# Optimization experiments

Measured on AMD Instinct MI355X. Metric: run time of the kernel, lower is better.

## Reference

```python
import jax, jax.numpy as jnp
import numpy as np

DIM = 1024
HEADS = 16
SEQ = 1024
BATCH = 4
SCALE = (DIM // HEADS) ** -0.5


def setup_inputs() -> dict:
    key = jax.random.key(0)
    ks = jax.random.split(key, 5)
    x = jax.random.normal(ks[0], (BATCH, SEQ, DIM), dtype=jnp.float32)
    # Linear weights stored [in, out]; y = x @ W + b (math-equivalent to torch Linear)
    w_qkv = jax.random.normal(ks[1], (DIM, 3 * DIM), dtype=jnp.float32) * (DIM ** -0.5)
    b_qkv = jnp.zeros((3 * DIM,), dtype=jnp.float32)
    w_proj = jax.random.normal(ks[2], (DIM, DIM), dtype=jnp.float32) * (DIM ** -0.5)
    b_proj = jnp.zeros((DIM,), dtype=jnp.float32)
    rel_table = jax.random.normal(ks[3], (2 * SEQ - 1, HEADS), dtype=jnp.float32) * 0.02
    coords = jnp.arange(SEQ)
    rel_index = (coords[:, None] - coords[None, :] + SEQ - 1).astype(jnp.int32)  # [N, N]
    return {"x": x, "w_qkv": w_qkv, "b_qkv": b_qkv, "w_proj": w_proj,
            "b_proj": b_proj, "rel_table": rel_table, "rel_index": rel_index}


def reference(x, w_qkv, b_qkv, w_proj, b_proj, rel_table, rel_index):
    B, N, C = x.shape
    H = HEADS
    hd = C // H
    qkv = (x @ w_qkv + b_qkv).reshape(B, N, 3, H, hd).transpose(2, 0, 3, 1, 4)  # [3,B,H,N,hd]
    q, k, v = qkv[0] * SCALE, qkv[1], qkv[2]
    attn = jnp.einsum('bhqe,bhke->bhqk', q, k)                 # [B,H,N,N]
    bias = rel_table[rel_index]                                 # [N,N,H] gather
    attn = attn + bias.transpose(2, 0, 1)[None]                 # add [1,H,N,N]
    attn = jax.nn.softmax(attn, axis=-1)
    # Faithful to the original einsum 'bnqk,bnqe->bnqe' (contracts k over attn only)
    out = jnp.einsum('bnqk,bnqe->bnqe', attn, v)                # [B,H,N,hd]
    out = out.transpose(0, 2, 1, 3).reshape(B, N, C)
    return out @ w_proj + b_proj
```

## Files before the change

kernel.cpp:

```cpp
#include <hip/hip_runtime.h>
#include <type_traits>


#define DIMC 1024
#define MTOT 4096

__device__ __forceinline__ unsigned short f2bf(float f) {
  unsigned u = __float_as_uint(f);
  u += 0x7FFFu + ((u >> 16) & 1u);
  return (unsigned short)(u >> 16);
}

typedef __attribute__((ext_vector_type(8))) short short8;
typedef __attribute__((ext_vector_type(4))) float floatx4;

__device__ __forceinline__ void async_copy16(const void* g, void* l) {
  __builtin_amdgcn_global_load_lds(
      (const __attribute__((address_space(1))) unsigned int*)g,
      (__attribute__((address_space(3))) unsigned int*)l,
      16, 0, 0);
}

__device__ __forceinline__ short8 cvt8(floatx4 lo, floatx4 hi) {
  unsigned r0, r1, r2, r3;
  asm("v_cvt_pk_bf16_f32 %0, %1, %2" : "=v"(r0) : "v"(lo[0]), "v"(lo[1]));
  asm("v_cvt_pk_bf16_f32 %0, %1, %2" : "=v"(r1) : "v"(lo[2]), "v"(lo[3]));
  asm("v_cvt_pk_bf16_f32 %0, %1, %2" : "=v"(r2) : "v"(hi[0]), "v"(hi[1]));
  asm("v_cvt_pk_bf16_f32 %0, %1, %2" : "=v"(r3) : "v"(hi[2]), "v"(hi[3]));
  union { unsigned u[4]; short8 s; } u;
  u.u[0] = r0; u.u[1] = r1; u.u[2] = r2; u.u[3] = r3;
  return u.s;
}

__global__ void prep_kernel(const float* __restrict__ w_proj,
                            const float* __restrict__ w_qkv,
                            const float* __restrict__ b_v,
                            unsigned short* __restrict__ WpT,
                            unsigned short* __restrict__ Wvb,
                            float* __restrict__ b_cp) {
  __shared__ float tile[32][33];
  const int t = threadIdx.x;
  const int tx = t & 31, ty = t >> 5;
  const int bx = blockIdx.x, by = blockIdx.y;
#pragma unroll
  for (int r = 0; r < 4; ++r) {
    int kl = ty + r * 8;
    tile[kl][tx] = w_proj[(size_t)(by * 32 + kl) * DIMC + bx * 32 + tx];
  }
  {
    const int r2 = t >> 3, c4 = (t & 7) * 4;
    float4 f = *(const float4*)(w_qkv + (size_t)(by * 32 + r2) * (3 * DIMC) +
                                2 * DIMC + bx * 32 + c4);
    ushort4 o;
    o.x = f2bf(f.x); o.y = f2bf(f.y); o.z = f2bf(f.z); o.w = f2bf(f.w);
    *(ushort4*)(Wvb + (size_t)(by * 32 + r2) * DIMC + bx * 32 + c4) = o;
  }
  __syncthreads();
#pragma unroll
  for (int r = 0; r < 4; ++r) {
    int nl = ty + r * 8;
    WpT[(size_t)(bx * 32 + nl) * DIMC + by * 32 + tx] = f2bf(tile[tx][nl]);
  }
  if (t < 32) {
    float s = 0.f;
#pragma unroll
    for (int kl = 0; kl < 32; ++kl) s += b_v[by * 32 + kl] * tile[kl][t];
    b_cp[(size_t)by * DIMC + bx * 32 + t] = s;
  }
}

template <int BM, int BN, bool AF32, bool BF16_OUT, bool SWZ>
__global__ __launch_bounds__(256) void gemm_bt_kernel(
    const void* __restrict__ A,
    const unsigned short* __restrict__ Bt,
    const float* __restrict__ bias,
    const float* __restrict__ bias2,
    void* __restrict__ Cout, int M, int N, int K, int gx,
    const float* __restrict__ bcp,
    float* __restrict__ bcred) {
  using AT = typename std::conditional<AF32, float, unsigned short>::type;
  constexpr int MI = BM / 32;
  constexpr int NI = BN / 32;
  constexpr int AG = AF32 ? BM / 16 : BM / 32;
  constexpr int BG = BN / 32;
  constexpr int ASZ = BM * 64 * (AF32 ? 4 : 2);
  __shared__ __align__(16) char Asb[2][ASZ];
  __shared__ __align__(16) unsigned short Bs[2][BN * 64];

  const AT* Ap = (const AT*)A;
  const int tid = threadIdx.x;
  const int wv = tid >> 6;
  const int lane = tid & 63;

  int bx, by;
  if (SWZ) {
    const int bid = blockIdx.x;
    bx = (bid >> 3) & 7;
    by = (bid & 7) * 4 + (bid >> 6);
  } else {
    bx = blockIdx.x % gx;
    by = blockIdx.x / gx;
  }
  const int m0 = by * BM;
  const int n0 = bx * BN;

  floatx4 acc[MI][NI] = {};

  const AT* Ag[AG];
  if constexpr (AF32) {
    const int srow = tid >> 4;
    const int skc = (tid & 15) ^ srow;
#pragma unroll
    for (int g = 0; g < AG; ++g)
      Ag[g] = Ap + (size_t)(m0 + g * 16 + srow) * K + skc * 4;
  } else {
    const int srow = tid >> 3;
    const int skc = (tid & 7) ^ (srow & 7);
#pragma unroll
    for (int g = 0; g < AG; ++g)
      Ag[g] = Ap + (size_t)(m0 + g * 32 + srow) * K + skc * 8;
  }
  const unsigned short* Bg[BG];
  {
    const int srow = tid >> 3;
    const int skc = (tid & 7) ^ (srow & 7);
#pragma unroll
    for (int g = 0; g < BG; ++g)
      Bg[g] = Bt + (size_t)(n0 + g * 32 + srow) * K + skc * 8;
  }

  const int lr = lane & 15;
  const int qr = lane >> 4;
  const int lx = lr & 7;
  const int wrow = (wv >> 1) * (BM / 2);
  const int wcol = (wv & 1) * (BN / 2);

  const int NT = K >> 6;

#pragma unroll
  for (int g = 0; g < AG; ++g)
    async_copy16(Ag[g], Asb[0] + g * 4096 + wv * 1024);
#pragma unroll
  for (int g = 0; g < BG; ++g)
    async_copy16(Bg[g], (char*)Bs[0] + g * 4096 + wv * 1024);
  asm volatile("s_waitcnt vmcnt(0)" ::: "memory");
  __builtin_amdgcn_s_barrier();

  int cur = 0;
  for (int t = 0; t < NT; ++t) {
    const char* Asc = Asb[cur];
    const unsigned short* Bsc = Bs[cur];
    const bool pre = (t + 1 < NT);
    if (pre) {
      const int nxt = cur ^ 1;
      const int kn = (t + 1) * 64;
#pragma unroll
      for (int g = 0; g < AG; ++g)
        async_copy16(Ag[g] + kn, Asb[nxt] + g * 4096 + wv * 1024);
#pragma unroll
      for (int g = 0; g < BG; ++g)
        async_copy16(Bg[g] + kn, (char*)Bs[nxt] + g * 4096 + wv * 1024);
    }

    short8 a[2][MI], b[2][NI];
#pragma unroll
    for (int s = 0; s < 2; ++s) {
#pragma unroll
      for (int mi = 0; mi < MI; ++mi) {
        const int row = wrow + mi * 16 + lr;
        if constexpr (AF32) {
          const float* Afl = (const float*)Asc;
          const int c0 = (s * 4 + qr) * 2;
          floatx4 lo = *(const floatx4*)(Afl + row * 64 + ((c0 ^ lr) * 4));
          floatx4 hi = *(const floatx4*)(Afl + row * 64 + (((c0 + 1) ^ lr) * 4));
          a[s][mi] = cvt8(lo, hi);
        } else {
          const unsigned short* Au = (const unsigned short*)Asc;
          const int kphys = ((s * 4 + qr) ^ lx) * 8;
          a[s][mi] = *(const short8*)(Au + row * 64 + kphys);
        }
      }
      const int kphysb = ((s * 4 + qr) ^ lx) * 8;
#pragma unroll
      for (int ni = 0; ni < NI; ++ni)
        b[s][ni] = *(const short8*)(Bsc + (wcol + ni * 16 + lr) * 64 + kphysb);
    }
#pragma unroll
    for (int s = 0; s < 2; ++s)
#pragma unroll
      for (int mi = 0; mi < MI; ++mi)
#pragma unroll
        for (int ni = 0; ni < NI; ++ni)
          acc[mi][ni] = __builtin_amdgcn_mfma_f32_16x16x32_bf16(a[s][mi], b[s][ni],
                                                                acc[mi][ni], 0, 0, 0);
    if (pre) {
      asm volatile("s_waitcnt vmcnt(0)" ::: "memory");
      __builtin_amdgcn_s_barrier();
    }
    cur ^= 1;
  }

#pragma unroll
  for (int mi = 0; mi < MI; ++mi) {
#pragma unroll
    for (int ni = 0; ni < NI; ++ni) {
      const int col = n0 + wcol + ni * 16 + lr;
      float bv = 0.0f;
      if (bias)  bv += bias[col];
      if (bias2) bv += bias2[col];
#pragma unroll
      for (int r = 0; r < 4; ++r) {
        const int row = m0 + wrow + mi * 16 + qr * 4 + r;
        const float val = acc[mi][ni][r] + bv;
        if (BF16_OUT)
          ((unsigned short*)Cout)[(size_t)row * N + col] = f2bf(val);
        else
          ((float*)Cout)[(size_t)row * N + col] = val;
      }
    }
  }

  if (bcp) {
    if (blockIdx.x < 16 && tid < 64) {
      const int col = blockIdx.x * 64 + tid;
      float ssum = 0.f;
#pragma unroll
      for (int p = 0; p < 32; ++p) ssum += bcp[p * DIMC + col];
      bcred[col] = ssum;
    }
  }
}

extern "C" void kernel_launch(void* const* d_in, const int* in_sizes, int n_in,
                              void* d_out, int out_size, void* d_ws, size_t ws_size,
                              hipStream_t stream) {
  const float* x      = (const float*)d_in[0];
  const float* w_qkv  = (const float*)d_in[1];
  const float* b_qkv  = (const float*)d_in[2];
  const float* w_proj = (const float*)d_in[3];
  const float* b_proj = (const float*)d_in[4];
  float* out = (float*)d_out;

  char* ws = (char*)d_ws;
  unsigned short* WpT = (unsigned short*)(ws);
  unsigned short* Wvb = (unsigned short*)(ws + (size_t)(2u << 20));
  unsigned short* WcT = (unsigned short*)(ws + (size_t)(4u << 20));
  float*          b_cp= (float*)(ws + (size_t)(6u << 20));
  float*          b_c = (float*)(ws + (size_t)(6u << 20) + 131072);

  prep_kernel<<<dim3(32, 32), 256, 0, stream>>>(w_proj, w_qkv, b_qkv + 2 * DIMC,
                                                WpT, Wvb, b_cp);
  gemm_bt_kernel<64, 64, false, true, false><<<256, 256, 0, stream>>>(
      WpT, Wvb, nullptr, nullptr, WcT, DIMC, DIMC, DIMC, DIMC / 64, b_cp, b_c);
  gemm_bt_kernel<128, 128, true, false, true><<<256, 256, 0, stream>>>(
      x, WcT, b_c, b_proj, out, MTOT, DIMC, DIMC, DIMC / 128, nullptr, nullptr);
}
```

Measured before the change: 130.3 us.

## Convert fp32 A tile to bf16 in registers before storing to LDS

The fp32 x operand was previously streamed into LDS with async global-to-LDS copies and converted to bf16 on every fragment read. It is now loaded into registers, converted once, and written to LDS as bf16 after the MFMA block. This halves LDS footprint and read traffic for A and removes repeated conversions across the warp tile. The cost is register staging with explicit loads and stores, and a __syncthreads in place of the raw barrier.

```diff
diff --git a/kernel.cpp b/kernel.cpp
--- a/kernel.cpp
+++ b/kernel.cpp
@@ -78,16 +78,13 @@
     void* __restrict__ Cout, int M, int N, int K, int gx,
     const float* __restrict__ bcp,
     float* __restrict__ bcred) {
-  using AT = typename std::conditional<AF32, float, unsigned short>::type;
   constexpr int MI = BM / 32;
   constexpr int NI = BN / 32;
-  constexpr int AG = AF32 ? BM / 16 : BM / 32;
+  constexpr int AG = BM / 32;
   constexpr int BG = BN / 32;
-  constexpr int ASZ = BM * 64 * (AF32 ? 4 : 2);
-  __shared__ __align__(16) char Asb[2][ASZ];
+  __shared__ __align__(16) unsigned short As[2][BM * 64];
   __shared__ __align__(16) unsigned short Bs[2][BN * 64];
 
-  const AT* Ap = (const AT*)A;
   const int tid = threadIdx.x;
   const int wv = tid >> 6;
   const int lane = tid & 63;
@@ -106,28 +103,30 @@
 
   floatx4 acc[MI][NI] = {};
 
-  const AT* Ag[AG];
+  const int srow = tid >> 3;
+  const int sc = tid & 7;
+  const int sx = srow & 7;
+
+  const float* Agf[AG];
+  const unsigned short* Agb[AG];
+  unsigned short* Awr[AG];
   if constexpr (AF32) {
-    const int srow = tid >> 4;
-    const int skc = (tid & 15) ^ srow;
+    const float* Ap = (const float*)A;
+#pragma unroll
+    for (int g = 0; g < AG; ++g) {
+      Agf[g] = Ap + (size_t)(m0 + g * 32 + srow) * K + sc * 8;
+      Awr[g] = (unsigned short*)0 + (g * 32 + srow) * 64 + (sc ^ sx) * 8;
+    }
+  } else {
+    const unsigned short* Ap = (const unsigned short*)A;
 #pragma unroll
     for (int g = 0; g < AG; ++g)
-      Ag[g] = Ap + (size_t)(m0 + g * 16 + srow) * K + skc * 4;
-  } else {
-    const int srow = tid >> 3;
-    const int skc = (tid & 7) ^ (srow & 7);
-#pragma unroll
-    for (int g = 0; g < AG; ++g)
-      Ag[g] = Ap + (size_t)(m0 + g * 32 + srow) * K + skc * 8;
+      Agb[g] = Ap + (size_t)(m0 + g * 32 + srow) * K + (sc ^ sx) * 8;
   }
   const unsigned short* Bg[BG];
-  {
-    const int srow = tid >> 3;
-    const int skc = (tid & 7) ^ (srow & 7);
-#pragma unroll
-    for (int g = 0; g < BG; ++g)
-      Bg[g] = Bt + (size_t)(n0 + g * 32 + srow) * K + skc * 8;
-  }
+#pragma unroll
+  for (int g = 0; g < BG; ++g)
+    Bg[g] = Bt + (size_t)(n0 + g * 32 + srow) * K + (sc ^ sx) * 8;
 
   const int lr = lane & 15;
   const int qr = lane >> 4;
@@ -137,26 +136,44 @@
 
   const int NT = K >> 6;
 
-#pragma unroll
-  for (int g = 0; g < AG; ++g)
-    async_copy16(Ag[g], Asb[0] + g * 4096 + wv * 1024);
+  if constexpr (AF32) {
+#pragma unroll
+    for (int g = 0; g < AG; ++g) {
+      floatx4 lo = *(const floatx4*)(Agf[g]);
+      floatx4 hi = *(const floatx4*)(Agf[g] + 4);
+      *(short8*)(As[0] + (size_t)(Awr[g] - (unsigned short*)0)) = cvt8(lo, hi);
+    }
+  } else {
+#pragma unroll
+    for (int g = 0; g < AG; ++g)
+      async_copy16(Agb[g], (char*)As[0] + g * 4096 + wv * 1024);
+  }
 #pragma unroll
   for (int g = 0; g < BG; ++g)
     async_copy16(Bg[g], (char*)Bs[0] + g * 4096 + wv * 1024);
-  asm volatile("s_waitcnt vmcnt(0)" ::: "memory");
-  __builtin_amdgcn_s_barrier();
+  __syncthreads();
 
   int cur = 0;
   for (int t = 0; t < NT; ++t) {
-    const char* Asc = Asb[cur];
+    const unsigned short* Asc = As[cur];
     const unsigned short* Bsc = Bs[cur];
     const bool pre = (t + 1 < NT);
+    const int nxt = cur ^ 1;
+    const int kn = (t + 1) * 64;
+
+    floatx4 alo[AG], ahi[AG];
     if (pre) {
-      const int nxt = cur ^ 1;
-      const int kn = (t + 1) * 64;
-#pragma unroll
-      for (int g = 0; g < AG; ++g)
-        async_copy16(Ag[g] + kn, Asb[nxt] + g * 4096 + wv * 1024);
+      if constexpr (AF32) {
+#pragma unroll
+        for (int g = 0; g < AG; ++g) {
+          alo[g] = *(const floatx4*)(Agf[g] + kn);
+          ahi[g] = *(const floatx4*)(Agf[g] + kn + 4);
+        }
+      } else {
+#pragma unroll
+        for (int g = 0; g < AG; ++g)
+          async_copy16(Agb[g] + kn, (char*)As[nxt] + g * 4096 + wv * 1024);
+      }
 #pragma unroll
       for (int g = 0; g < BG; ++g)
         async_copy16(Bg[g] + kn, (char*)Bs[nxt] + g * 4096 + wv * 1024);
@@ -165,25 +182,13 @@
     short8 a[2][MI], b[2][NI];
 #pragma unroll
     for (int s = 0; s < 2; ++s) {
-#pragma unroll
-      for (int mi = 0; mi < MI; ++mi) {
-        const int row = wrow + mi * 16 + lr;
-        if constexpr (AF32) {
-          const float* Afl = (const float*)Asc;
-          const int c0 = (s * 4 + qr) * 2;
-          floatx4 lo = *(const floatx4*)(Afl + row * 64 + ((c0 ^ lr) * 4));
-          floatx4 hi = *(const floatx4*)(Afl + row * 64 + (((c0 + 1) ^ lr) * 4));
-          a[s][mi] = cvt8(lo, hi);
-        } else {
-          const unsigned short* Au = (const unsigned short*)Asc;
-          const int kphys = ((s * 4 + qr) ^ lx) * 8;
-          a[s][mi] = *(const short8*)(Au + row * 64 + kphys);
-        }
-      }
-      const int kphysb = ((s * 4 + qr) ^ lx) * 8;
+      const int kphys = ((s * 4 + qr) ^ lx) * 8;
+#pragma unroll
+      for (int mi = 0; mi < MI; ++mi)
+        a[s][mi] = *(const short8*)(Asc + (wrow + mi * 16 + lr) * 64 + kphys);
 #pragma unroll
       for (int ni = 0; ni < NI; ++ni)
-        b[s][ni] = *(const short8*)(Bsc + (wcol + ni * 16 + lr) * 64 + kphysb);
+        b[s][ni] = *(const short8*)(Bsc + (wcol + ni * 16 + lr) * 64 + kphys);
     }
 #pragma unroll
     for (int s = 0; s < 2; ++s)
@@ -194,8 +199,13 @@
           acc[mi][ni] = __builtin_amdgcn_mfma_f32_16x16x32_bf16(a[s][mi], b[s][ni],
                                                                 acc[mi][ni], 0, 0, 0);
     if (pre) {
-      asm volatile("s_waitcnt vmcnt(0)" ::: "memory");
-      __builtin_amdgcn_s_barrier();
+      if constexpr (AF32) {
+#pragma unroll
+        for (int g = 0; g < AG; ++g)
+          *(short8*)(As[nxt] + (size_t)(Awr[g] - (unsigned short*)0)) =
+              cvt8(alo[g], ahi[g]);
+      }
+      __syncthreads();
     }
     cur ^= 1;
   }
```

New measurement: 128.4 us. Within noise of the previous version (-1.5%).
